# Kernel tuning notes

Hardware: AMD Instinct MI355X
Metric: run time of the kernel (lower is better)

The kernel has to match this reference:

```python
import jax, jax.numpy as jnp
import numpy as np

EPS = 1e-5

def _layernorm(x, g, b):
    m = jnp.mean(x, axis=-1, keepdims=True)
    v = jnp.mean((x - m) ** 2, axis=-1, keepdims=True)
    return (x - m) * jax.lax.rsqrt(v + EPS) * g + b

def setup_inputs() -> dict:
    N, D, R = 1024, 128, 64
    dist_mean = 60.0
    key = jax.random.key(0)
    ks = jax.random.split(key, 12)
    def lin(k, fan_in, shape):
        bound = 1.0 / np.sqrt(fan_in)
        return jax.random.uniform(k, shape, jnp.float32, -bound, bound)
    inp = {
        "node_emb": jax.random.normal(ks[0], (N, D), jnp.float32),
        # src_proj: Linear(D, R) + LayerNorm(R)
        "w_src": lin(ks[1], D, (R, D)), "b_src": lin(ks[2], D, (R,)),
        "g_src": jnp.ones((R,), jnp.float32), "be_src": jnp.zeros((R,), jnp.float32),
        # dst_proj: Linear(D, R) + LayerNorm(R)
        "w_dst": lin(ks[3], D, (R, D)), "b_dst": lin(ks[4], D, (R,)),
        "g_dst": jnp.ones((R,), jnp.float32), "be_dst": jnp.zeros((R,), jnp.float32),
        # scorer: Linear(3R, 2R) -> ReLU -> Linear(2R, R) -> ReLU -> Linear(R, 1)
        "w1": lin(ks[5], 3 * R, (2 * R, 3 * R)), "b1": lin(ks[6], 3 * R, (2 * R,)),
        "w2": lin(ks[7], 2 * R, (R, 2 * R)), "b2": lin(ks[8], 2 * R, (R,)),
        "w3": lin(ks[9], R, (1, R)) * 0.01, "b3": jnp.full((1,), dist_mean, jnp.float32),
    }
    return inp

def reference(node_emb, w_src, b_src, g_src, be_src, w_dst, b_dst, g_dst, be_dst,
              w1, b1, w2, b2, w3, b3):
    # src/dst projections: [N, R]
    src = jax.nn.relu(_layernorm(node_emb @ w_src.T + b_src, g_src, be_src))
    dst = jax.nn.relu(_layernorm(node_emb @ w_dst.T + b_dst, g_dst, be_dst))
    N = node_emb.shape[0]
    # broadcast pairwise features: [N, N, 3R]
    src_exp = jnp.broadcast_to(src[:, None, :], (N, N, src.shape[-1]))
    dst_exp = jnp.broadcast_to(dst[None, :, :], (N, N, dst.shape[-1]))
    pair = jnp.concatenate([src_exp, dst_exp, src_exp * dst_exp], axis=-1)
    h = jax.nn.relu(pair @ w1.T + b1)   # [N, N, 2R]
    h = jax.nn.relu(h @ w2.T + b2)      # [N, N, R]
    cost = (h @ w3.T + b3)[..., 0]      # [N, N]
    return cost
```

## Files before the change

### kernel.cpp

```cpp
#include <hip/hip_runtime.h>

typedef _Float16 half2v __attribute__((ext_vector_type(2)));
typedef _Float16 half8v __attribute__((ext_vector_type(8)));
typedef float f32x4 __attribute__((ext_vector_type(4)));
typedef unsigned uint2v __attribute__((ext_vector_type(2)));

__device__ inline half2v cvt_pk(float a, float b) {
    return __builtin_bit_cast(half2v, __builtin_amdgcn_cvt_pkrtz(a, b));
}
__device__ inline half2v pkmax0(half2v x) {
    half2v r;
    asm("v_pk_max_f16 %0, %1, 0" : "=v"(r) : "v"(x));
    return r;
}
__device__ inline unsigned short f16bits(float f) {
    _Float16 h = (_Float16)f;
    return __builtin_bit_cast(unsigned short, h);
}
__device__ inline unsigned packf16(float a, float b) {
    return (unsigned)f16bits(a) | ((unsigned)f16bits(b) << 16);
}
__device__ inline float lo16(unsigned u) {
    return (float)__builtin_bit_cast(_Float16, (unsigned short)(u & 0xffffu));
}
__device__ inline float hi16(unsigned u) {
    return (float)__builtin_bit_cast(_Float16, (unsigned short)(u >> 16));
}

__global__ __launch_bounds__(256) void proj_kernel(
    const float* __restrict__ node,
    const float* __restrict__ w_src, const float* __restrict__ b_src,
    const float* __restrict__ g_src, const float* __restrict__ be_src,
    const float* __restrict__ w_dst, const float* __restrict__ b_dst,
    const float* __restrict__ g_dst, const float* __restrict__ be_dst,
    const float* __restrict__ w1, const float* __restrict__ b1,
    const float* __restrict__ w2,
    unsigned short* __restrict__ src_f16, unsigned short* __restrict__ dst_f16,
    float* __restrict__ A1, unsigned short* __restrict__ B1h,
    unsigned short* __restrict__ w1c_frag, unsigned short* __restrict__ w2_frag)
{
    __shared__ unsigned sWh[64 * 65];
    __shared__ unsigned sw1h[128 * 33];
    __shared__ float snode[4][128];
    __shared__ float sy[4][64];

    const int tid = threadIdx.x;
    const int wloc = tid >> 6;
    const int lane = tid & 63;
    const int gw = blockIdx.x * 4 + wloc;
    const int row = gw & 1023;
    const int kind = gw >> 10;

    const float* W  = kind ? w_dst  : w_src;
    const float* Bv = kind ? b_dst  : b_src;
    const float* G  = kind ? g_dst  : g_src;
    const float* BE = kind ? be_dst : be_src;
    const int koff = kind * 64;

    #pragma unroll
    for (int u = 0; u < 16; u++) {
        int w = u * 256 + tid;
        int r = w >> 6, c2 = w & 63;
        float2 v = *(const float2*)(W + r * 128 + c2 * 2);
        sWh[r * 65 + c2] = packf16(v.x, v.y);
    }
    #pragma unroll
    for (int u = 0; u < 16; u++) {
        int w = u * 256 + tid;
        int r = w >> 5, c2 = w & 31;
        float2 v = *(const float2*)(w1 + (size_t)r * 192 + koff + c2 * 2);
        sw1h[r * 33 + c2] = packf16(v.x, v.y);
    }
    snode[wloc][lane]      = node[row * 128 + lane];
    snode[wloc][lane + 64] = node[row * 128 + 64 + lane];
    __syncthreads();

    float acc = Bv[lane];
    #pragma unroll 8
    for (int k2 = 0; k2 < 64; k2++) {
        unsigned wp = sWh[lane * 65 + k2];
        float2 nv = *(const float2*)&snode[wloc][2 * k2];
        acc += nv.x * lo16(wp) + nv.y * hi16(wp);
    }

    float s = acc;
    #pragma unroll
    for (int off = 32; off >= 1; off >>= 1) s += __shfl_xor(s, off);
    float mean = s * (1.0f / 64.0f);
    float d = acc - mean;
    float ss = d * d;
    #pragma unroll
    for (int off = 32; off >= 1; off >>= 1) ss += __shfl_xor(ss, off);
    float rstd = rsqrtf(ss * (1.0f / 64.0f) + 1e-5f);
    float y = fmaxf(d * rstd * G[lane] + BE[lane], 0.0f);

    unsigned short* obf = kind ? dst_f16 : src_f16;
    obf[row * 64 + lane] = f16bits(y);

    sy[wloc][lane] = y;
    __builtin_amdgcn_s_waitcnt(0);

    float a0 = kind ? 0.0f : b1[lane];
    float a1 = kind ? 0.0f : b1[lane + 64];
    #pragma unroll 8
    for (int k2 = 0; k2 < 32; k2++) {
        float2 yv = *(const float2*)&sy[wloc][2 * k2];
        unsigned wa = sw1h[lane * 33 + k2];
        unsigned wb = sw1h[(lane + 64) * 33 + k2];
        a0 += yv.x * lo16(wa) + yv.y * hi16(wa);
        a1 += yv.x * lo16(wb) + yv.y * hi16(wb);
    }
    if (kind == 0) {
        A1[row * 128 + lane] = a0;
        A1[row * 128 + lane + 64] = a1;
    } else {
        B1h[row * 128 + lane] = f16bits(a0);
        B1h[row * 128 + lane + 64] = f16bits(a1);
    }

    if (blockIdx.x < 8) {
        int t = blockIdx.x * 256 + threadIdx.x;
        int which = t >> 10;
        int idx = t & 1023;
        int f = idx >> 6, l = idx & 63;
        int lqq = l >> 4, lrr = l & 15;
        if (which == 0) {
            int mt = f >> 1, kt = f & 1;
            #pragma unroll
            for (int e = 0; e < 8; e++)
                w1c_frag[idx * 8 + e] =
                    f16bits(w1[(size_t)(mt * 16 + lrr) * 192 + 128 + kt * 32 + lqq * 8 + e]);
        } else {
            int mt2 = f >> 2, kt2 = f & 3;
            #pragma unroll
            for (int e = 0; e < 8; e++) {
                int col = (2 * kt2 + (e >> 2)) * 16 + lqq * 4 + (e & 3);
                w2_frag[idx * 8 + e] =
                    f16bits(w2[(size_t)(mt2 * 16 + lrr) * 128 + col]);
            }
        }
    }
}

__global__ __launch_bounds__(256, 2) void pair_kernel(
    const unsigned short* __restrict__ src_f16, const unsigned short* __restrict__ dst_f16,
    const float* __restrict__ A1, const unsigned short* __restrict__ B1h,
    const unsigned short* __restrict__ w1c_frag, const unsigned short* __restrict__ w2_frag,
    const float* __restrict__ b2, const float* __restrict__ w3,
    const float* __restrict__ b3, float* __restrict__ out)
{
    __shared__ __align__(16) float sA1[32][128];
    __shared__ __align__(16) unsigned short sSrc[32][64];
    __shared__ __align__(16) unsigned short sB1[32][136];
    __shared__ __align__(16) float sB2[128];
    __shared__ __align__(16) float sW3[64];

    const int tid = threadIdx.x;
    const int wv = tid >> 6;
    const int lane = tid & 63;
    const int lq = lane >> 4, lr = lane & 15;
    const int i0 = blockIdx.y * 32, j0 = blockIdx.x * 32;
    const int ibase = (wv & 1) * 16;
    const int jl_base = (wv >> 1) * 16;
    const int jbase = j0 + jl_base;

    #pragma unroll
    for (int u = 0; u < 4; u++) {
        int idx = u * 256 + tid;
        int r = idx >> 5, c = (idx & 31) * 4;
        *(f32x4*)&sA1[r][c] = *(const f32x4*)(A1 + (size_t)(i0 + r) * 128 + c);
    }
    {
        int r = tid >> 3, c = (tid & 7) * 8;
        *(uint4*)&sSrc[r][c] = *(const uint4*)(src_f16 + (size_t)(i0 + r) * 64 + c);
    }
    #pragma unroll
    for (int u = 0; u < 2; u++) {
        int idx = u * 256 + tid;
        int r = idx >> 4, c = (idx & 15) * 8;
        *(uint4*)&sB1[r][c] = *(const uint4*)(B1h + (size_t)(j0 + r) * 128 + c);
    }
    if (tid < 32) *(f32x4*)&sB2[tid * 4] = *(const f32x4*)(b2 + tid * 4);
    else if (tid < 48) *(f32x4*)&sW3[(tid - 32) * 4] = *(const f32x4*)(w3 + (tid - 32) * 4);

    half8v w1f[8][2], w2f[4][4];
    {
        const uint4* gw1 = (const uint4*)w1c_frag;
        #pragma unroll
        for (int mt = 0; mt < 8; mt++)
            #pragma unroll
            for (int kt = 0; kt < 2; kt++)
                w1f[mt][kt] = __builtin_bit_cast(half8v, gw1[(mt * 2 + kt) * 64 + lane]);
        const uint4* gw2 = (const uint4*)w2_frag;
        #pragma unroll
        for (int mt2 = 0; mt2 < 4; mt2++)
            #pragma unroll
            for (int kt = 0; kt < 4; kt++)
                w2f[mt2][kt] = __builtin_bit_cast(half8v, gw2[(mt2 * 4 + kt) * 64 + lane]);
    }
    const float b3s = b3[0];

    const int j = jbase + lr;
    half8v dstf0, dstf1;
    {
        const uint4* drow = (const uint4*)(dst_f16 + (size_t)j * 64);
        dstf0 = __builtin_bit_cast(half8v, drow[lq]);
        dstf1 = __builtin_bit_cast(half8v, drow[4 + lq]);
    }
    const int jl = jl_base + lr;

    __syncthreads();

    for (int cc = 0; cc < 16; cc++) {
        const int i_loc = ibase + cc;
        const int i = i0 + i_loc;
        const half8v s0 = *(const half8v*)&sSrc[i_loc][lq * 8];
        const half8v s1 = *(const half8v*)&sSrc[i_loc][32 + lq * 8];
        f32x4 acc1[8];
        #pragma unroll
        for (int mt = 0; mt < 8; mt++)
            acc1[mt] = *(const f32x4*)&sA1[i_loc][mt * 16 + lq * 4];
        const half8v c0 = s0 * dstf0;
        const half8v c1 = s1 * dstf1;
        #pragma unroll
        for (int mt = 0; mt < 8; mt++) {
            acc1[mt] = __builtin_amdgcn_mfma_f32_16x16x32_f16(w1f[mt][0], c0, acc1[mt], 0, 0, 0);
            acc1[mt] = __builtin_amdgcn_mfma_f32_16x16x32_f16(w1f[mt][1], c1, acc1[mt], 0, 0, 0);
        }
        unsigned P[16];
        #pragma unroll
        for (int mt = 0; mt < 8; mt++) {
            uint2v bl = *(const uint2v*)&sB1[jl][mt * 16 + lq * 4];
            half2v p0 = cvt_pk(acc1[mt][0], acc1[mt][1]) + __builtin_bit_cast(half2v, bl[0]);
            half2v p1 = cvt_pk(acc1[mt][2], acc1[mt][3]) + __builtin_bit_cast(half2v, bl[1]);
            P[mt * 2 + 0] = __builtin_bit_cast(unsigned, pkmax0(p0));
            P[mt * 2 + 1] = __builtin_bit_cast(unsigned, pkmax0(p1));
        }
        f32x4 acc2[4];
        {
            uint4 hb = {P[0], P[1], P[2], P[3]};
            half8v hf = __builtin_bit_cast(half8v, hb);
            #pragma unroll
            for (int mt2 = 0; mt2 < 4; mt2++) {
                f32x4 b2t = *(const f32x4*)&sB2[mt2 * 16 + lq * 4];
                acc2[mt2] = __builtin_amdgcn_mfma_f32_16x16x32_f16(w2f[mt2][0], hf, b2t, 0, 0, 0);
            }
        }
        #pragma unroll
        for (int kt = 1; kt < 4; kt++) {
            uint4 hb = {P[4 * kt], P[4 * kt + 1], P[4 * kt + 2], P[4 * kt + 3]};
            half8v hf = __builtin_bit_cast(half8v, hb);
            #pragma unroll
            for (int mt2 = 0; mt2 < 4; mt2++)
                acc2[mt2] = __builtin_amdgcn_mfma_f32_16x16x32_f16(w2f[mt2][kt], hf, acc2[mt2], 0, 0, 0);
        }
        float part = 0.0f;
        #pragma unroll
        for (int mt2 = 0; mt2 < 4; mt2++) {
            f32x4 w3t = *(const f32x4*)&sW3[mt2 * 16 + lq * 4];
            #pragma unroll
            for (int r = 0; r < 4; r++)
                part += fmaxf(acc2[mt2][r], 0.0f) * w3t[r];
        }
        part += __shfl_xor(part, 16);
        part += __shfl_xor(part, 32);
        if (lane < 16)
            out[(size_t)i * 1024 + jbase + lane] = part + b3s;
    }
}

extern "C" void kernel_launch(void* const* d_in, const int* in_sizes, int n_in,
                              void* d_out, int out_size, void* d_ws, size_t ws_size,
                              hipStream_t stream) {
    (void)in_sizes; (void)n_in; (void)out_size; (void)ws_size;
    const float* node   = (const float*)d_in[0];
    const float* w_src  = (const float*)d_in[1];
    const float* b_src  = (const float*)d_in[2];
    const float* g_src  = (const float*)d_in[3];
    const float* be_src = (const float*)d_in[4];
    const float* w_dst  = (const float*)d_in[5];
    const float* b_dst  = (const float*)d_in[6];
    const float* g_dst  = (const float*)d_in[7];
    const float* be_dst = (const float*)d_in[8];
    const float* w1     = (const float*)d_in[9];
    const float* b1     = (const float*)d_in[10];
    const float* w2     = (const float*)d_in[11];
    const float* b2     = (const float*)d_in[12];
    const float* w3     = (const float*)d_in[13];
    const float* b3     = (const float*)d_in[14];

    char* ws = (char*)d_ws;
    unsigned short* src_f16  = (unsigned short*)(ws);
    unsigned short* dst_f16  = (unsigned short*)(ws + 131072);
    float*          A1       = (float*)(ws + 262144);
    unsigned short* B1h      = (unsigned short*)(ws + 786432);
    unsigned short* w1c_frag = (unsigned short*)(ws + 1310720);
    unsigned short* w2_frag  = (unsigned short*)(ws + 1327104);

    hipLaunchKernelGGL(proj_kernel, dim3(512), dim3(256), 0, stream,
                       node, w_src, b_src, g_src, be_src, w_dst, b_dst, g_dst, be_dst,
                       w1, b1, w2, src_f16, dst_f16, A1, B1h,
                       w1c_frag, w2_frag);
    hipLaunchKernelGGL(pair_kernel, dim3(32, 32), dim3(256), 0, stream,
                       src_f16, dst_f16, A1, B1h, w1c_frag, w2_frag, b2, w3, b3,
                       (float*)d_out);
}
```

Before: 46.22 us.

## Switch pair kernel to 32x32x16 MFMA tiles with per-wave i-row split

```diff
diff --git a/kernel.cpp b/kernel.cpp
--- a/kernel.cpp
+++ b/kernel.cpp
@@ -3,6 +3,7 @@
 typedef _Float16 half2v __attribute__((ext_vector_type(2)));
 typedef _Float16 half8v __attribute__((ext_vector_type(8)));
 typedef float f32x4 __attribute__((ext_vector_type(4)));
+typedef float f32x16 __attribute__((ext_vector_type(16)));
 typedef unsigned uint2v __attribute__((ext_vector_type(2)));
 
 __device__ inline half2v cvt_pk(float a, float b) {
@@ -123,20 +124,20 @@
         int which = t >> 10;
         int idx = t & 1023;
         int f = idx >> 6, l = idx & 63;
-        int lqq = l >> 4, lrr = l & 15;
+        int lrow = l & 31, lhi = l >> 5;
         if (which == 0) {
-            int mt = f >> 1, kt = f & 1;
+            int mt = f >> 2, kt = f & 3;
             #pragma unroll
             for (int e = 0; e < 8; e++)
                 w1c_frag[idx * 8 + e] =
-                    f16bits(w1[(size_t)(mt * 16 + lrr) * 192 + 128 + kt * 32 + lqq * 8 + e]);
+                    f16bits(w1[(size_t)(32 * mt + lrow) * 192 + 128 + 16 * kt + 8 * lhi + e]);
         } else {
-            int mt2 = f >> 2, kt2 = f & 3;
+            int mt2 = f >> 3, b = f & 7;
             #pragma unroll
             for (int e = 0; e < 8; e++) {
-                int col = (2 * kt2 + (e >> 2)) * 16 + lqq * 4 + (e & 3);
+                int col = 16 * b + 4 * lhi + (e >> 2) * 8 + (e & 3);
                 w2_frag[idx * 8 + e] =
-                    f16bits(w2[(size_t)(mt2 * 16 + lrr) * 128 + col]);
+                    f16bits(w2[(size_t)(32 * mt2 + lrow) * 128 + col]);
             }
         }
     }
@@ -151,18 +152,15 @@
 {
     __shared__ __align__(16) float sA1[32][128];
     __shared__ __align__(16) unsigned short sSrc[32][64];
-    __shared__ __align__(16) unsigned short sB1[32][136];
     __shared__ __align__(16) float sB2[128];
     __shared__ __align__(16) float sW3[64];
 
     const int tid = threadIdx.x;
     const int wv = tid >> 6;
     const int lane = tid & 63;
-    const int lq = lane >> 4, lr = lane & 15;
+    const int hi = lane >> 5, col = lane & 31;
     const int i0 = blockIdx.y * 32, j0 = blockIdx.x * 32;
-    const int ibase = (wv & 1) * 16;
-    const int jl_base = (wv >> 1) * 16;
-    const int jbase = j0 + jl_base;
+    const int ibase = wv * 8;
 
     #pragma unroll
     for (int u = 0; u < 4; u++) {
@@ -174,98 +172,105 @@
         int r = tid >> 3, c = (tid & 7) * 8;
         *(uint4*)&sSrc[r][c] = *(const uint4*)(src_f16 + (size_t)(i0 + r) * 64 + c);
     }
-    #pragma unroll
-    for (int u = 0; u < 2; u++) {
-        int idx = u * 256 + tid;
-        int r = idx >> 4, c = (idx & 15) * 8;
-        *(uint4*)&sB1[r][c] = *(const uint4*)(B1h + (size_t)(j0 + r) * 128 + c);
-    }
     if (tid < 32) *(f32x4*)&sB2[tid * 4] = *(const f32x4*)(b2 + tid * 4);
     else if (tid < 48) *(f32x4*)&sW3[(tid - 32) * 4] = *(const f32x4*)(w3 + (tid - 32) * 4);
 
-    half8v w1f[8][2], w2f[4][4];
-    {
-        const uint4* gw1 = (const uint4*)w1c_frag;
-        #pragma unroll
-        for (int mt = 0; mt < 8; mt++)
-            #pragma unroll
-            for (int kt = 0; kt < 2; kt++)
-                w1f[mt][kt] = __builtin_bit_cast(half8v, gw1[(mt * 2 + kt) * 64 + lane]);
-        const uint4* gw2 = (const uint4*)w2_frag;
-        #pragma unroll
-        for (int mt2 = 0; mt2 < 4; mt2++)
-            #pragma unroll
-            for (int kt = 0; kt < 4; kt++)
-                w2f[mt2][kt] = __builtin_bit_cast(half8v, gw2[(mt2 * 4 + kt) * 64 + lane]);
-    }
+    const int j = j0 + col;
+    half8v dstf[4];
+    #pragma unroll
+    for (int kt = 0; kt < 4; kt++)
+        dstf[kt] = *(const half8v*)(dst_f16 + (size_t)j * 64 + 16 * kt + 8 * hi);
+    unsigned b1pk[4][8];
+    #pragma unroll
+    for (int mt = 0; mt < 4; mt++)
+        #pragma unroll
+        for (int t = 0; t < 8; t++) {
+            int x = ((2 * t) & 3) + 8 * (t >> 1) + 4 * hi;
+            b1pk[mt][t] = *(const unsigned*)(B1h + (size_t)j * 128 + 32 * mt + x);
+        }
     const float b3s = b3[0];
 
-    const int j = jbase + lr;
-    half8v dstf0, dstf1;
-    {
-        const uint4* drow = (const uint4*)(dst_f16 + (size_t)j * 64);
-        dstf0 = __builtin_bit_cast(half8v, drow[lq]);
-        dstf1 = __builtin_bit_cast(half8v, drow[4 + lq]);
-    }
-    const int jl = jl_base + lr;
+    const uint4* gw1 = (const uint4*)w1c_frag;
+    const uint4* gw2 = (const uint4*)w2_frag;
 
     __syncthreads();
 
-    for (int cc = 0; cc < 16; cc++) {
+    #pragma unroll 2
+    for (int cc = 0; cc < 8; cc++) {
         const int i_loc = ibase + cc;
         const int i = i0 + i_loc;
-        const half8v s0 = *(const half8v*)&sSrc[i_loc][lq * 8];
-        const half8v s1 = *(const half8v*)&sSrc[i_loc][32 + lq * 8];
-        f32x4 acc1[8];
-        #pragma unroll
-        for (int mt = 0; mt < 8; mt++)
-            acc1[mt] = *(const f32x4*)&sA1[i_loc][mt * 16 + lq * 4];
-        const half8v c0 = s0 * dstf0;
-        const half8v c1 = s1 * dstf1;
-        #pragma unroll
-        for (int mt = 0; mt < 8; mt++) {
-            acc1[mt] = __builtin_amdgcn_mfma_f32_16x16x32_f16(w1f[mt][0], c0, acc1[mt], 0, 0, 0);
-            acc1[mt] = __builtin_amdgcn_mfma_f32_16x16x32_f16(w1f[mt][1], c1, acc1[mt], 0, 0, 0);
+
+        half8v cf[4];
+        #pragma unroll
+        for (int kt = 0; kt < 4; kt++)
+            cf[kt] = (*(const half8v*)&sSrc[i_loc][16 * kt + 8 * hi]) * dstf[kt];
+
+        f32x16 acc1[4];
+        #pragma unroll
+        for (int mt = 0; mt < 4; mt++)
+            #pragma unroll
+            for (int s = 0; s < 4; s++) {
+                f32x4 v = *(const f32x4*)&sA1[i_loc][32 * mt + 8 * s + 4 * hi];
+                acc1[mt][4 * s + 0] = v[0];
+                acc1[mt][4 * s + 1] = v[1];
+                acc1[mt][4 * s + 2] = v[2];
+                acc1[mt][4 * s + 3] = v[3];
+            }
+
+        #pragma unroll
+        for (int kt = 0; kt < 4; kt++)
+            #pragma unroll
+            for (int mt = 0; mt < 4; mt++) {
+                half8v wf = __builtin_bit_cast(half8v, gw1[(mt * 4 + kt) * 64 + lane]);
+                acc1[mt] = __builtin_amdgcn_mfma_f32_32x32x16_f16(wf, cf[kt], acc1[mt], 0, 0, 0);
+            }
+
+        unsigned P[4][8];
+        #pragma unroll
+        for (int mt = 0; mt < 4; mt++)
+            #pragma unroll
+            for (int t = 0; t < 8; t++) {
+                half2v p = cvt_pk(acc1[mt][2 * t], acc1[mt][2 * t + 1])
+                         + __builtin_bit_cast(half2v, b1pk[mt][t]);
+                P[mt][t] = __builtin_bit_cast(unsigned, pkmax0(p));
+            }
+
+        f32x16 acc2[2];
+        #pragma unroll
+        for (int mt2 = 0; mt2 < 2; mt2++)
+            #pragma unroll
+            for (int s = 0; s < 4; s++) {
+                f32x4 v = *(const f32x4*)&sB2[32 * mt2 + 8 * s + 4 * hi];
+                acc2[mt2][4 * s + 0] = v[0];
+                acc2[mt2][4 * s + 1] = v[1];
+                acc2[mt2][4 * s + 2] = v[2];
+                acc2[mt2][4 * s + 3] = v[3];
+            }
+        #pragma unroll
+        for (int b = 0; b < 8; b++) {
+            const int mt = b >> 1, h = b & 1;
+            uint4 hb = {P[mt][4 * h], P[mt][4 * h + 1], P[mt][4 * h + 2], P[mt][4 * h + 3]};
+            half8v hf = __builtin_bit_cast(half8v, hb);
+            #pragma unroll
+            for (int mt2 = 0; mt2 < 2; mt2++) {
+                half8v wf = __builtin_bit_cast(half8v, gw2[(mt2 * 8 + b) * 64 + lane]);
+                acc2[mt2] = __builtin_amdgcn_mfma_f32_32x32x16_f16(wf, hf, acc2[mt2], 0, 0, 0);
+            }
         }
-        unsigned P[16];
-        #pragma unroll
-        for (int mt = 0; mt < 8; mt++) {
-            uint2v bl = *(const uint2v*)&sB1[jl][mt * 16 + lq * 4];
-            half2v p0 = cvt_pk(acc1[mt][0], acc1[mt][1]) + __builtin_bit_cast(half2v, bl[0]);
-            half2v p1 = cvt_pk(acc1[mt][2], acc1[mt][3]) + __builtin_bit_cast(half2v, bl[1]);
-            P[mt * 2 + 0] = __builtin_bit_cast(unsigned, pkmax0(p0));
-            P[mt * 2 + 1] = __builtin_bit_cast(unsigned, pkmax0(p1));
-        }
-        f32x4 acc2[4];
-        {
-            uint4 hb = {P[0], P[1], P[2], P[3]};
-            half8v hf = __builtin_bit_cast(half8v, hb);
-            #pragma unroll
-            for (int mt2 = 0; mt2 < 4; mt2++) {
-                f32x4 b2t = *(const f32x4*)&sB2[mt2 * 16 + lq * 4];
-                acc2[mt2] = __builtin_amdgcn_mfma_f32_16x16x32_f16(w2f[mt2][0], hf, b2t, 0, 0, 0);
-            }
-        }
-        #pragma unroll
-        for (int kt = 1; kt < 4; kt++) {
-            uint4 hb = {P[4 * kt], P[4 * kt + 1], P[4 * kt + 2], P[4 * kt + 3]};
-            half8v hf = __builtin_bit_cast(half8v, hb);
-            #pragma unroll
-            for (int mt2 = 0; mt2 < 4; mt2++)
-                acc2[mt2] = __builtin_amdgcn_mfma_f32_16x16x32_f16(w2f[mt2][kt], hf, acc2[mt2], 0, 0, 0);
-        }
+
         float part = 0.0f;
         #pragma unroll
-        for (int mt2 = 0; mt2 < 4; mt2++) {
-            f32x4 w3t = *(const f32x4*)&sW3[mt2 * 16 + lq * 4];
-            #pragma unroll
-            for (int r = 0; r < 4; r++)
-                part += fmaxf(acc2[mt2][r], 0.0f) * w3t[r];
-        }
-        part += __shfl_xor(part, 16);
+        for (int mt2 = 0; mt2 < 2; mt2++)
+            #pragma unroll
+            for (int s = 0; s < 4; s++) {
+                f32x4 w3t = *(const f32x4*)&sW3[32 * mt2 + 8 * s + 4 * hi];
+                #pragma unroll
+                for (int q = 0; q < 4; q++)
+                    part += fmaxf(acc2[mt2][4 * s + q], 0.0f) * w3t[q];
+            }
         part += __shfl_xor(part, 32);
-        if (lane < 16)
-            out[(size_t)i * 1024 + jbase + lane] = part + b3s;
+        if (lane < 32)
+            out[(size_t)i * 1024 + j0 + col] = part + b3s;
     }
 }
 
```

New measurement: 159.6 us. 245% more time.
